# Optimization experiments

Hardware: AMD Instinct MI355X
Metric: run time of the kernel (lower is better)

Reference implementation:

```python
import jax, jax.numpy as jnp
import numpy as np

IN_DIM = 32768
OUT_DIM = 32768
BATCH = 1024


def setup_inputs() -> dict:
    key = jax.random.key(0)
    k1, k2, k3, k4 = jax.random.split(key, 4)
    x = jax.random.uniform(k1, (BATCH, IN_DIM), dtype=jnp.float32)
    negation_logits = jax.random.normal(k2, (OUT_DIM, 2), dtype=jnp.float32)
    idx_a = jax.random.randint(k3, (OUT_DIM,), 0, IN_DIM, dtype=jnp.int64)
    idx_b = jax.random.randint(k4, (OUT_DIM,), 0, IN_DIM, dtype=jnp.int64)
    return {"x": x, "negation_logits": negation_logits, "idx_a": idx_a, "idx_b": idx_b}


def reference(x, negation_logits, idx_a, idx_b):
    # Gather the two fan-in wires of every AND gate: [B, out_dim]
    a = x[:, idx_a]
    b = x[:, idx_b]
    # Hard negation flags from learned logits (straight-through: forward value is hard).
    p = jax.nn.sigmoid(negation_logits)  # [out_dim, 2]
    flag = p > 0.5
    a_mod = jnp.where(flag[:, 0][None, :], 1.0 - a, a)
    b_mod = jnp.where(flag[:, 1][None, :], 1.0 - b, b)
    return a_mod * b_mod  # soft AND gate
```

## Files before the change

kernel.cpp:

```cpp
#include <hip/hip_runtime.h>
#include <stdint.h>

#define IN_DIM  32768
#define OUT_DIM 32768
#define BATCH   1024
#define NT      1024
#define ITER    (OUT_DIM / 4 / NT)

typedef float fvec4 __attribute__((ext_vector_type(4)));

__device__ __forceinline__ uint32_t f32_to_bf16_bits(float f) {
    uint32_t u = __builtin_bit_cast(uint32_t, f);
    return (u + 0x7FFFu + ((u >> 16) & 1u)) >> 16;
}

__global__ void pack_meta(const int* __restrict__ idx_a,
                          const int* __restrict__ idx_b,
                          const float* __restrict__ logits,
                          uint32_t* __restrict__ packed) {
    int j = blockIdx.x * blockDim.x + threadIdx.x;
    if (j >= OUT_DIM) return;
    uint32_t ia = (((uint32_t)idx_a[j]) << 1) & 0xFFFFu;
    uint32_t ib = (((uint32_t)idx_b[j]) << 1) & 0xFFFFu;
    if (logits[2 * j + 0] > 0.0f) ia |= 1u;
    if (logits[2 * j + 1] > 0.0f) ib |= 1u;
    packed[j] = ia | (ib << 16);
}

__device__ __forceinline__ float ldrow(const uint16_t* row, uint32_t byteoff) {
    uint16_t h = *(const uint16_t*)((const char*)row + byteoff);
    return __builtin_bit_cast(float, ((uint32_t)h) << 16);
}
__device__ __forceinline__ float sel(uint32_t flag, float v) {
    return flag ? 1.0f - v : v;
}

__global__ __launch_bounds__(NT, 8) void logic_gather(
        const float* __restrict__ x,
        const uint32_t* __restrict__ packed,
        float* __restrict__ out) {
    __shared__ __align__(16) uint16_t row[IN_DIM];
    const int r = blockIdx.x;
    const int t = threadIdx.x;

    const float4* __restrict__ xrow = (const float4*)(x + (size_t)r * IN_DIM);
    uint2* __restrict__ row64 = (uint2*)row;
#pragma unroll
    for (int i = 0; i < IN_DIM / 4 / NT; ++i) {
        int e4 = i * NT + t;
        float4 v = xrow[e4];
        uint2 h;
        h.x = f32_to_bf16_bits(v.x) | (f32_to_bf16_bits(v.y) << 16);
        h.y = f32_to_bf16_bits(v.z) | (f32_to_bf16_bits(v.w) << 16);
        row64[e4] = h;
    }

    const uint4* __restrict__ pk = (const uint4*)packed;
    uint4 p[ITER];
#pragma unroll
    for (int i = 0; i < ITER; ++i) p[i] = pk[i * NT + t];

    __syncthreads();

    fvec4* __restrict__ orow = (fvec4*)(out + (size_t)r * OUT_DIM);
#pragma unroll
    for (int i = 0; i < ITER; ++i) {
        const uint32_t w0 = p[i].x, w1 = p[i].y, w2 = p[i].z, w3 = p[i].w;
        float a0 = ldrow(row, w0 & 0xFFFEu), b0 = ldrow(row, (w0 >> 16) & 0xFFFEu);
        float a1 = ldrow(row, w1 & 0xFFFEu), b1 = ldrow(row, (w1 >> 16) & 0xFFFEu);
        float a2 = ldrow(row, w2 & 0xFFFEu), b2 = ldrow(row, (w2 >> 16) & 0xFFFEu);
        float a3 = ldrow(row, w3 & 0xFFFEu), b3 = ldrow(row, (w3 >> 16) & 0xFFFEu);
        fvec4 res;
        res.x = sel(w0 & 1u, a0) * sel(w0 & 0x10000u, b0);
        res.y = sel(w1 & 1u, a1) * sel(w1 & 0x10000u, b1);
        res.z = sel(w2 & 1u, a2) * sel(w2 & 0x10000u, b2);
        res.w = sel(w3 & 1u, a3) * sel(w3 & 0x10000u, b3);
        __builtin_nontemporal_store(res, &orow[i * NT + t]);
    }
}

extern "C" void kernel_launch(void* const* d_in, const int* in_sizes, int n_in,
                              void* d_out, int out_size, void* d_ws, size_t ws_size,
                              hipStream_t stream) {
    const float* x      = (const float*)d_in[0];
    const float* logits = (const float*)d_in[1];
    const int*   idx_a  = (const int*)d_in[2];
    const int*   idx_b  = (const int*)d_in[3];
    uint32_t*    packed = (uint32_t*)d_ws;
    float*       out    = (float*)d_out;

    hipLaunchKernelGGL(pack_meta, dim3(OUT_DIM / 256), dim3(256), 0, stream,
                       idx_a, idx_b, logits, packed);
    hipLaunchKernelGGL(logic_gather, dim3(BATCH), dim3(NT), 0, stream,
                       x, packed, out);
}
```

Baseline: 243.5 us.

## Process two rows per block, prefetch next row during gather, use fp16 staging

Each block now handles two batch rows. While it gathers and stores the first row from shared memory, it prefetches the second row's x data into registers, so the global load latency overlaps with compute and the output stores. The shared-row conversion changes from a manual bf16 round-to-nearest to the hardware packed fp16 round-toward-zero conversion, which is cheaper to compute. The change adds extra barriers, raises register pressure from the eight prefetched float4 values, and halves the grid size. The fp16 conversion also changes rounding and precision; inputs in [0,1) fit fp16 well.

```diff
diff --git a/kernel.cpp b/kernel.cpp
--- a/kernel.cpp
+++ b/kernel.cpp
@@ -6,12 +6,22 @@
 #define BATCH   1024
 #define NT      1024
 #define ITER    (OUT_DIM / 4 / NT)
+#define SITER   (IN_DIM / 4 / NT)
+#define RPB     2
+#define GRID    (BATCH / RPB)
 
 typedef float fvec4 __attribute__((ext_vector_type(4)));
 
-__device__ __forceinline__ uint32_t f32_to_bf16_bits(float f) {
-    uint32_t u = __builtin_bit_cast(uint32_t, f);
-    return (u + 0x7FFFu + ((u >> 16) & 1u)) >> 16;
+__device__ __forceinline__ uint32_t pack2_f16(float lo, float hi) {
+    auto h = __builtin_amdgcn_cvt_pkrtz(lo, hi);
+    return __builtin_bit_cast(uint32_t, h);
+}
+__device__ __forceinline__ float ldrow(const uint16_t* row, uint32_t byteoff) {
+    _Float16 h = *(const _Float16*)((const char*)row + byteoff);
+    return (float)h;
+}
+__device__ __forceinline__ float sel(uint32_t flag, float v) {
+    return flag ? 1.0f - v : v;
 }
 
 __global__ void pack_meta(const int* __restrict__ idx_a,
@@ -27,56 +37,93 @@
     packed[j] = ia | (ib << 16);
 }
 
-__device__ __forceinline__ float ldrow(const uint16_t* row, uint32_t byteoff) {
-    uint16_t h = *(const uint16_t*)((const char*)row + byteoff);
-    return __builtin_bit_cast(float, ((uint32_t)h) << 16);
-}
-__device__ __forceinline__ float sel(uint32_t flag, float v) {
-    return flag ? 1.0f - v : v;
-}
-
 __global__ __launch_bounds__(NT, 8) void logic_gather(
         const float* __restrict__ x,
         const uint32_t* __restrict__ packed,
         float* __restrict__ out) {
     __shared__ __align__(16) uint16_t row[IN_DIM];
-    const int r = blockIdx.x;
-    const int t = threadIdx.x;
+    const int t  = threadIdx.x;
+    const int r0 = blockIdx.x;
+    const int r1 = r0 + GRID;
 
-    const float4* __restrict__ xrow = (const float4*)(x + (size_t)r * IN_DIM);
-    uint2* __restrict__ row64 = (uint2*)row;
+    const uint4* __restrict__ pk    = (const uint4*)packed;
+    uint2*       __restrict__ row64 = (uint2*)row;
+
+    {
+        const float4* __restrict__ xr = (const float4*)(x + (size_t)r0 * IN_DIM);
 #pragma unroll
-    for (int i = 0; i < IN_DIM / 4 / NT; ++i) {
-        int e4 = i * NT + t;
-        float4 v = xrow[e4];
-        uint2 h;
-        h.x = f32_to_bf16_bits(v.x) | (f32_to_bf16_bits(v.y) << 16);
-        h.y = f32_to_bf16_bits(v.z) | (f32_to_bf16_bits(v.w) << 16);
-        row64[e4] = h;
+        for (int i = 0; i < SITER; ++i) {
+            float4 v = xr[i * NT + t];
+            uint2 h;
+            h.x = pack2_f16(v.x, v.y);
+            h.y = pack2_f16(v.z, v.w);
+            row64[i * NT + t] = h;
+        }
+    }
+    __syncthreads();
+
+    const float4* __restrict__ xr1 = (const float4*)(x + (size_t)r1 * IN_DIM);
+    float4 pf0, pf1, pf2, pf3, pf4, pf5, pf6, pf7;
+
+#define STEP(i, orow, ...)                                                          \
+    {                                                                               \
+        uint4 p1 = ((i) + 1 < ITER) ? pk[((i) + 1) * NT + t] : p0;                  \
+        __VA_ARGS__;                                                                \
+        const uint32_t w0 = p0.x, w1 = p0.y, w2 = p0.z, w3 = p0.w;                  \
+        float a0 = ldrow(row, w0 & 0xFFFEu), b0 = ldrow(row, (w0 >> 16) & 0xFFFEu); \
+        float a1 = ldrow(row, w1 & 0xFFFEu), b1 = ldrow(row, (w1 >> 16) & 0xFFFEu); \
+        float a2 = ldrow(row, w2 & 0xFFFEu), b2 = ldrow(row, (w2 >> 16) & 0xFFFEu); \
+        float a3 = ldrow(row, w3 & 0xFFFEu), b3 = ldrow(row, (w3 >> 16) & 0xFFFEu); \
+        fvec4 res;                                                                  \
+        res.x = sel(w0 & 1u, a0) * sel(w0 & 0x10000u, b0);                          \
+        res.y = sel(w1 & 1u, a1) * sel(w1 & 0x10000u, b1);                          \
+        res.z = sel(w2 & 1u, a2) * sel(w2 & 0x10000u, b2);                          \
+        res.w = sel(w3 & 1u, a3) * sel(w3 & 0x10000u, b3);                          \
+        __builtin_nontemporal_store(res, &(orow)[(i) * NT + t]);                    \
+        p0 = p1;                                                                    \
     }
 
-    const uint4* __restrict__ pk = (const uint4*)packed;
-    uint4 p[ITER];
-#pragma unroll
-    for (int i = 0; i < ITER; ++i) p[i] = pk[i * NT + t];
+    {
+        fvec4* __restrict__ o0 = (fvec4*)(out + (size_t)r0 * OUT_DIM);
+        uint4 p0 = pk[t];
+        STEP(0, o0, __builtin_amdgcn_sched_barrier(0); pf0 = xr1[0 * NT + t])
+        STEP(1, o0, __builtin_amdgcn_sched_barrier(0); pf1 = xr1[1 * NT + t])
+        STEP(2, o0, __builtin_amdgcn_sched_barrier(0); pf2 = xr1[2 * NT + t])
+        STEP(3, o0, __builtin_amdgcn_sched_barrier(0); pf3 = xr1[3 * NT + t])
+        STEP(4, o0, __builtin_amdgcn_sched_barrier(0); pf4 = xr1[4 * NT + t])
+        STEP(5, o0, __builtin_amdgcn_sched_barrier(0); pf5 = xr1[5 * NT + t])
+        STEP(6, o0, __builtin_amdgcn_sched_barrier(0); pf6 = xr1[6 * NT + t])
+        STEP(7, o0, __builtin_amdgcn_sched_barrier(0); pf7 = xr1[7 * NT + t])
+    }
 
     __syncthreads();
 
-    fvec4* __restrict__ orow = (fvec4*)(out + (size_t)r * OUT_DIM);
-#pragma unroll
-    for (int i = 0; i < ITER; ++i) {
-        const uint32_t w0 = p[i].x, w1 = p[i].y, w2 = p[i].z, w3 = p[i].w;
-        float a0 = ldrow(row, w0 & 0xFFFEu), b0 = ldrow(row, (w0 >> 16) & 0xFFFEu);
-        float a1 = ldrow(row, w1 & 0xFFFEu), b1 = ldrow(row, (w1 >> 16) & 0xFFFEu);
-        float a2 = ldrow(row, w2 & 0xFFFEu), b2 = ldrow(row, (w2 >> 16) & 0xFFFEu);
-        float a3 = ldrow(row, w3 & 0xFFFEu), b3 = ldrow(row, (w3 >> 16) & 0xFFFEu);
-        fvec4 res;
-        res.x = sel(w0 & 1u, a0) * sel(w0 & 0x10000u, b0);
-        res.y = sel(w1 & 1u, a1) * sel(w1 & 0x10000u, b1);
-        res.z = sel(w2 & 1u, a2) * sel(w2 & 0x10000u, b2);
-        res.w = sel(w3 & 1u, a3) * sel(w3 & 0x10000u, b3);
-        __builtin_nontemporal_store(res, &orow[i * NT + t]);
+    {
+        uint2 h;
+        h.x = pack2_f16(pf0.x, pf0.y); h.y = pack2_f16(pf0.z, pf0.w); row64[0 * NT + t] = h;
+        h.x = pack2_f16(pf1.x, pf1.y); h.y = pack2_f16(pf1.z, pf1.w); row64[1 * NT + t] = h;
+        h.x = pack2_f16(pf2.x, pf2.y); h.y = pack2_f16(pf2.z, pf2.w); row64[2 * NT + t] = h;
+        h.x = pack2_f16(pf3.x, pf3.y); h.y = pack2_f16(pf3.z, pf3.w); row64[3 * NT + t] = h;
+        h.x = pack2_f16(pf4.x, pf4.y); h.y = pack2_f16(pf4.z, pf4.w); row64[4 * NT + t] = h;
+        h.x = pack2_f16(pf5.x, pf5.y); h.y = pack2_f16(pf5.z, pf5.w); row64[5 * NT + t] = h;
+        h.x = pack2_f16(pf6.x, pf6.y); h.y = pack2_f16(pf6.z, pf6.w); row64[6 * NT + t] = h;
+        h.x = pack2_f16(pf7.x, pf7.y); h.y = pack2_f16(pf7.z, pf7.w); row64[7 * NT + t] = h;
     }
+    __syncthreads();
+
+    {
+        fvec4* __restrict__ o1 = (fvec4*)(out + (size_t)r1 * OUT_DIM);
+        uint4 p0 = pk[t];
+        STEP(0, o1)
+        STEP(1, o1)
+        STEP(2, o1)
+        STEP(3, o1)
+        STEP(4, o1)
+        STEP(5, o1)
+        STEP(6, o1)
+        STEP(7, o1)
+    }
+#undef STEP
 }
 
 extern "C" void kernel_launch(void* const* d_in, const int* in_sizes, int n_in,
@@ -91,6 +138,6 @@
 
     hipLaunchKernelGGL(pack_meta, dim3(OUT_DIM / 256), dim3(256), 0, stream,
                        idx_a, idx_b, logits, packed);
-    hipLaunchKernelGGL(logic_gather, dim3(BATCH), dim3(NT), 0, stream,
+    hipLaunchKernelGGL(logic_gather, dim3(GRID), dim3(NT), 0, stream,
                        x, packed, out);
 }
```

Result: no change. 243.3 us (-0.1%).

## Process two batch rows per block with interleaved fp16 LDS row

Applied to the files above, without the earlier changes.

Each block now handles two batch rows. Both rows are stored interleaved as packed fp16 pairs in a 128 KB dynamic LDS buffer, so a single 32-bit LDS read fetches the value for both rows. This halves the number of blocks and the per-row reloads of the packed index metadata, and halves the gather LDS reads per output. In exchange, precision moves from bf16 to fp16 with round-toward-zero, occupancy per CU drops because of the larger LDS footprint, and a dynamic shared memory opt-in attribute is added.

```diff
diff --git a/kernel.cpp b/kernel.cpp
--- a/kernel.cpp
+++ b/kernel.cpp
@@ -6,12 +6,26 @@
 #define BATCH   1024
 #define NT      1024
 #define ITER    (OUT_DIM / 4 / NT)
+#define SITER   (IN_DIM / 4 / NT)
+#define RPB     2
+#define GRID    (BATCH / RPB)
+#define LDS_BYTES (IN_DIM * 4)
 
-typedef float fvec4 __attribute__((ext_vector_type(4)));
+typedef float  fvec4 __attribute__((ext_vector_type(4)));
+typedef __fp16 h2    __attribute__((ext_vector_type(2)));
 
-__device__ __forceinline__ uint32_t f32_to_bf16_bits(float f) {
-    uint32_t u = __builtin_bit_cast(uint32_t, f);
-    return (u + 0x7FFFu + ((u >> 16) & 1u)) >> 16;
+__device__ __forceinline__ uint32_t pack2_f16(float lo, float hi) {
+    h2 h = __builtin_amdgcn_cvt_pkrtz(lo, hi);
+    return __builtin_bit_cast(uint32_t, h);
+}
+__device__ __forceinline__ uint32_t ldw(const uint32_t* base, uint32_t byteoff) {
+    return *(const uint32_t*)((const char*)base + byteoff);
+}
+__device__ __forceinline__ uint32_t sel2(uint32_t flag, uint32_t w) {
+    h2 v = __builtin_bit_cast(h2, w);
+    h2 one; one.x = (__fp16)1.0f; one.y = (__fp16)1.0f;
+    h2 r = one - v;
+    return flag ? __builtin_bit_cast(uint32_t, r) : w;
 }
 
 __global__ void pack_meta(const int* __restrict__ idx_a,
@@ -27,32 +41,31 @@
     packed[j] = ia | (ib << 16);
 }
 
-__device__ __forceinline__ float ldrow(const uint16_t* row, uint32_t byteoff) {
-    uint16_t h = *(const uint16_t*)((const char*)row + byteoff);
-    return __builtin_bit_cast(float, ((uint32_t)h) << 16);
-}
-__device__ __forceinline__ float sel(uint32_t flag, float v) {
-    return flag ? 1.0f - v : v;
-}
-
-__global__ __launch_bounds__(NT, 8) void logic_gather(
+__global__ __launch_bounds__(NT, 4) void logic_gather(
         const float* __restrict__ x,
         const uint32_t* __restrict__ packed,
         float* __restrict__ out) {
-    __shared__ __align__(16) uint16_t row[IN_DIM];
-    const int r = blockIdx.x;
-    const int t = threadIdx.x;
+    extern __shared__ __align__(16) uint32_t rowi[];
+    const int t  = threadIdx.x;
+    const int r0 = blockIdx.x;
+    const int r1 = r0 + GRID;
 
-    const float4* __restrict__ xrow = (const float4*)(x + (size_t)r * IN_DIM);
-    uint2* __restrict__ row64 = (uint2*)row;
+    {
+        const float4* __restrict__ xr0 = (const float4*)(x + (size_t)r0 * IN_DIM);
+        const float4* __restrict__ xr1 = (const float4*)(x + (size_t)r1 * IN_DIM);
+        uint4* __restrict__ row128 = (uint4*)rowi;
 #pragma unroll
-    for (int i = 0; i < IN_DIM / 4 / NT; ++i) {
-        int e4 = i * NT + t;
-        float4 v = xrow[e4];
-        uint2 h;
-        h.x = f32_to_bf16_bits(v.x) | (f32_to_bf16_bits(v.y) << 16);
-        h.y = f32_to_bf16_bits(v.z) | (f32_to_bf16_bits(v.w) << 16);
-        row64[e4] = h;
+        for (int s = 0; s < SITER; ++s) {
+            int e4 = s * NT + t;
+            float4 v0 = xr0[e4];
+            float4 v1 = xr1[e4];
+            uint4 w;
+            w.x = pack2_f16(v0.x, v1.x);
+            w.y = pack2_f16(v0.y, v1.y);
+            w.z = pack2_f16(v0.z, v1.z);
+            w.w = pack2_f16(v0.w, v1.w);
+            row128[e4] = w;
+        }
     }
 
     const uint4* __restrict__ pk = (const uint4*)packed;
@@ -62,20 +75,30 @@
 
     __syncthreads();
 
-    fvec4* __restrict__ orow = (fvec4*)(out + (size_t)r * OUT_DIM);
+    fvec4* __restrict__ o0 = (fvec4*)(out + (size_t)r0 * OUT_DIM);
+    fvec4* __restrict__ o1 = (fvec4*)(out + (size_t)r1 * OUT_DIM);
+
 #pragma unroll
     for (int i = 0; i < ITER; ++i) {
         const uint32_t w0 = p[i].x, w1 = p[i].y, w2 = p[i].z, w3 = p[i].w;
-        float a0 = ldrow(row, w0 & 0xFFFEu), b0 = ldrow(row, (w0 >> 16) & 0xFFFEu);
-        float a1 = ldrow(row, w1 & 0xFFFEu), b1 = ldrow(row, (w1 >> 16) & 0xFFFEu);
-        float a2 = ldrow(row, w2 & 0xFFFEu), b2 = ldrow(row, (w2 >> 16) & 0xFFFEu);
-        float a3 = ldrow(row, w3 & 0xFFFEu), b3 = ldrow(row, (w3 >> 16) & 0xFFFEu);
-        fvec4 res;
-        res.x = sel(w0 & 1u, a0) * sel(w0 & 0x10000u, b0);
-        res.y = sel(w1 & 1u, a1) * sel(w1 & 0x10000u, b1);
-        res.z = sel(w2 & 1u, a2) * sel(w2 & 0x10000u, b2);
-        res.w = sel(w3 & 1u, a3) * sel(w3 & 0x10000u, b3);
-        __builtin_nontemporal_store(res, &orow[i * NT + t]);
+        uint32_t A0 = ldw(rowi, (w0 & 0xFFFEu) << 1), B0 = ldw(rowi, (w0 >> 15) & 0x1FFFCu);
+        uint32_t A1 = ldw(rowi, (w1 & 0xFFFEu) << 1), B1 = ldw(rowi, (w1 >> 15) & 0x1FFFCu);
+        uint32_t A2 = ldw(rowi, (w2 & 0xFFFEu) << 1), B2 = ldw(rowi, (w2 >> 15) & 0x1FFFCu);
+        uint32_t A3 = ldw(rowi, (w3 & 0xFFFEu) << 1), B3 = ldw(rowi, (w3 >> 15) & 0x1FFFCu);
+
+        h2 a0 = __builtin_bit_cast(h2, sel2(w0 & 1u, A0)), b0 = __builtin_bit_cast(h2, sel2(w0 & 0x10000u, B0));
+        h2 a1 = __builtin_bit_cast(h2, sel2(w1 & 1u, A1)), b1 = __builtin_bit_cast(h2, sel2(w1 & 0x10000u, B1));
+        h2 a2 = __builtin_bit_cast(h2, sel2(w2 & 1u, A2)), b2 = __builtin_bit_cast(h2, sel2(w2 & 0x10000u, B2));
+        h2 a3 = __builtin_bit_cast(h2, sel2(w3 & 1u, A3)), b3 = __builtin_bit_cast(h2, sel2(w3 & 0x10000u, B3));
+
+        fvec4 res0, res1;
+        res0.x = (float)a0.x * (float)b0.x;  res1.x = (float)a0.y * (float)b0.y;
+        res0.y = (float)a1.x * (float)b1.x;  res1.y = (float)a1.y * (float)b1.y;
+        res0.z = (float)a2.x * (float)b2.x;  res1.z = (float)a2.y * (float)b2.y;
+        res0.w = (float)a3.x * (float)b3.x;  res1.w = (float)a3.y * (float)b3.y;
+
+        __builtin_nontemporal_store(res0, &o0[i * NT + t]);
+        __builtin_nontemporal_store(res1, &o1[i * NT + t]);
     }
 }
 
@@ -89,8 +112,15 @@
     uint32_t*    packed = (uint32_t*)d_ws;
     float*       out    = (float*)d_out;
 
+    static bool lds_opt_in = false;
+    if (!lds_opt_in) {
+        (void)hipFuncSetAttribute(reinterpret_cast<const void*>(logic_gather),
+                                  hipFuncAttributeMaxDynamicSharedMemorySize, LDS_BYTES);
+        lds_opt_in = true;
+    }
+
     hipLaunchKernelGGL(pack_meta, dim3(OUT_DIM / 256), dim3(256), 0, stream,
                        idx_a, idx_b, logits, packed);
-    hipLaunchKernelGGL(logic_gather, dim3(BATCH), dim3(NT), 0, stream,
+    hipLaunchKernelGGL(logic_gather, dim3(GRID), dim3(NT), LDS_BYTES, stream,
                        x, packed, out);
 }
```

Result: no change. 245.6 us (+0.9%).

## Persistent blocks with double-buffered LDS rows and fp16 staging

Applied to the files above, without the earlier changes.

Cuts the grid to 256 blocks that each process four batch rows. The next row of x is prefetched into registers while the current row is gathered from LDS, then written into a second LDS buffer, so global loads overlap the gather and store work. The packed metadata is loaded once per block instead of once per row, and the bf16 conversion is replaced with a hardware fp16 packed round-toward-zero conversion. In exchange, LDS per block doubles to 128KB, occupancy is lower, and fp16 with truncating rounding changes numerical precision.

```diff
diff --git a/kernel.cpp b/kernel.cpp
--- a/kernel.cpp
+++ b/kernel.cpp
@@ -5,13 +5,25 @@
 #define OUT_DIM 32768
 #define BATCH   1024
 #define NT      1024
+#define GRID    256
+#define RPB     (BATCH / GRID)
 #define ITER    (OUT_DIM / 4 / NT)
+#define SITER   (IN_DIM / 4 / NT)
+#define LDS_BYTES (2 * IN_DIM * 2)
 
-typedef float fvec4 __attribute__((ext_vector_type(4)));
+typedef float  fvec4 __attribute__((ext_vector_type(4)));
+typedef __fp16 h2v   __attribute__((ext_vector_type(2)));
 
-__device__ __forceinline__ uint32_t f32_to_bf16_bits(float f) {
-    uint32_t u = __builtin_bit_cast(uint32_t, f);
-    return (u + 0x7FFFu + ((u >> 16) & 1u)) >> 16;
+__device__ __forceinline__ uint32_t pack2_f16(float lo, float hi) {
+    h2v h = __builtin_amdgcn_cvt_pkrtz(lo, hi);
+    return __builtin_bit_cast(uint32_t, h);
+}
+__device__ __forceinline__ float ldrow(const uint16_t* row, uint32_t byteoff) {
+    __fp16 h = *(const __fp16*)((const char*)row + byteoff);
+    return (float)h;
+}
+__device__ __forceinline__ float sel(uint32_t flag, float v) {
+    return flag ? 1.0f - v : v;
 }
 
 __global__ void pack_meta(const int* __restrict__ idx_a,
@@ -27,55 +39,76 @@
     packed[j] = ia | (ib << 16);
 }
 
-__device__ __forceinline__ float ldrow(const uint16_t* row, uint32_t byteoff) {
-    uint16_t h = *(const uint16_t*)((const char*)row + byteoff);
-    return __builtin_bit_cast(float, ((uint32_t)h) << 16);
-}
-__device__ __forceinline__ float sel(uint32_t flag, float v) {
-    return flag ? 1.0f - v : v;
-}
-
-__global__ __launch_bounds__(NT, 8) void logic_gather(
+__global__ __launch_bounds__(NT, 4) void logic_gather(
         const float* __restrict__ x,
         const uint32_t* __restrict__ packed,
         float* __restrict__ out) {
-    __shared__ __align__(16) uint16_t row[IN_DIM];
-    const int r = blockIdx.x;
+    extern __shared__ __align__(16) uint16_t lds[];
+    uint16_t* const buf0 = lds;
+    uint16_t* const buf1 = lds + IN_DIM;
     const int t = threadIdx.x;
-
-    const float4* __restrict__ xrow = (const float4*)(x + (size_t)r * IN_DIM);
-    uint2* __restrict__ row64 = (uint2*)row;
-#pragma unroll
-    for (int i = 0; i < IN_DIM / 4 / NT; ++i) {
-        int e4 = i * NT + t;
-        float4 v = xrow[e4];
-        uint2 h;
-        h.x = f32_to_bf16_bits(v.x) | (f32_to_bf16_bits(v.y) << 16);
-        h.y = f32_to_bf16_bits(v.z) | (f32_to_bf16_bits(v.w) << 16);
-        row64[e4] = h;
-    }
+    const int b = blockIdx.x;
 
     const uint4* __restrict__ pk = (const uint4*)packed;
     uint4 p[ITER];
 #pragma unroll
     for (int i = 0; i < ITER; ++i) p[i] = pk[i * NT + t];
 
+    {
+        const float4* __restrict__ xr = (const float4*)(x + (size_t)b * IN_DIM);
+        uint2* __restrict__ w64 = (uint2*)buf0;
+#pragma unroll
+        for (int s = 0; s < SITER; ++s) {
+            float4 v = xr[s * NT + t];
+            uint2 h;
+            h.x = pack2_f16(v.x, v.y);
+            h.y = pack2_f16(v.z, v.w);
+            w64[s * NT + t] = h;
+        }
+    }
     __syncthreads();
 
-    fvec4* __restrict__ orow = (fvec4*)(out + (size_t)r * OUT_DIM);
 #pragma unroll
-    for (int i = 0; i < ITER; ++i) {
-        const uint32_t w0 = p[i].x, w1 = p[i].y, w2 = p[i].z, w3 = p[i].w;
-        float a0 = ldrow(row, w0 & 0xFFFEu), b0 = ldrow(row, (w0 >> 16) & 0xFFFEu);
-        float a1 = ldrow(row, w1 & 0xFFFEu), b1 = ldrow(row, (w1 >> 16) & 0xFFFEu);
-        float a2 = ldrow(row, w2 & 0xFFFEu), b2 = ldrow(row, (w2 >> 16) & 0xFFFEu);
-        float a3 = ldrow(row, w3 & 0xFFFEu), b3 = ldrow(row, (w3 >> 16) & 0xFFFEu);
-        fvec4 res;
-        res.x = sel(w0 & 1u, a0) * sel(w0 & 0x10000u, b0);
-        res.y = sel(w1 & 1u, a1) * sel(w1 & 0x10000u, b1);
-        res.z = sel(w2 & 1u, a2) * sel(w2 & 0x10000u, b2);
-        res.w = sel(w3 & 1u, a3) * sel(w3 & 0x10000u, b3);
-        __builtin_nontemporal_store(res, &orow[i * NT + t]);
+    for (int k = 0; k < RPB; ++k) {
+        const uint16_t* __restrict__ cur = (k & 1) ? buf1 : buf0;
+        uint16_t*       __restrict__ nxt = (k & 1) ? buf0 : buf1;
+
+        float4 pf[SITER];
+        if (k + 1 < RPB) {
+            const float4* __restrict__ xr =
+                (const float4*)(x + (size_t)(b + (k + 1) * GRID) * IN_DIM);
+#pragma unroll
+            for (int s = 0; s < SITER; ++s) pf[s] = xr[s * NT + t];
+        }
+        __builtin_amdgcn_sched_barrier(0);
+
+        fvec4* __restrict__ o = (fvec4*)(out + (size_t)(b + k * GRID) * OUT_DIM);
+#pragma unroll
+        for (int i = 0; i < ITER; ++i) {
+            const uint32_t w0 = p[i].x, w1 = p[i].y, w2 = p[i].z, w3 = p[i].w;
+            float a0 = ldrow(cur, w0 & 0xFFFEu), b0 = ldrow(cur, (w0 >> 16) & 0xFFFEu);
+            float a1 = ldrow(cur, w1 & 0xFFFEu), b1 = ldrow(cur, (w1 >> 16) & 0xFFFEu);
+            float a2 = ldrow(cur, w2 & 0xFFFEu), b2 = ldrow(cur, (w2 >> 16) & 0xFFFEu);
+            float a3 = ldrow(cur, w3 & 0xFFFEu), b3 = ldrow(cur, (w3 >> 16) & 0xFFFEu);
+            fvec4 res;
+            res.x = sel(w0 & 1u, a0) * sel(w0 & 0x10000u, b0);
+            res.y = sel(w1 & 1u, a1) * sel(w1 & 0x10000u, b1);
+            res.z = sel(w2 & 1u, a2) * sel(w2 & 0x10000u, b2);
+            res.w = sel(w3 & 1u, a3) * sel(w3 & 0x10000u, b3);
+            __builtin_nontemporal_store(res, &o[i * NT + t]);
+        }
+
+        if (k + 1 < RPB) {
+            uint2* __restrict__ w64 = (uint2*)nxt;
+#pragma unroll
+            for (int s = 0; s < SITER; ++s) {
+                uint2 h;
+                h.x = pack2_f16(pf[s].x, pf[s].y);
+                h.y = pack2_f16(pf[s].z, pf[s].w);
+                w64[s * NT + t] = h;
+            }
+        }
+        __syncthreads();
     }
 }
 
@@ -89,8 +122,15 @@
     uint32_t*    packed = (uint32_t*)d_ws;
     float*       out    = (float*)d_out;
 
+    static bool lds_opt_in = false;
+    if (!lds_opt_in) {
+        (void)hipFuncSetAttribute(reinterpret_cast<const void*>(logic_gather),
+                                  hipFuncAttributeMaxDynamicSharedMemorySize, LDS_BYTES);
+        lds_opt_in = true;
+    }
+
     hipLaunchKernelGGL(pack_meta, dim3(OUT_DIM / 256), dim3(256), 0, stream,
                        idx_a, idx_b, logits, packed);
-    hipLaunchKernelGGL(logic_gather, dim3(BATCH), dim3(NT), 0, stream,
+    hipLaunchKernelGGL(logic_gather, dim3(GRID), dim3(NT), LDS_BYTES, stream,
                        x, packed, out);
 }
```

Result: slower. 254.1 us (+4.4%).
